# Performance work log

Hardware: AMD Instinct MI355X
Metric: run time of the kernel (lower is better)

## Reference

```python
import jax, jax.numpy as jnp
import numpy as np
from jax import lax

# ---- dims / config (see init_kwargs) ----
M_IMG, N_PCD, C = 1008, 1024, 256     # coarse img nodes (24*32+12*16+6*8), coarse pcd nodes, feat dim
NI_F, NP_F = 76800, 30000             # fine img pixels (240*320), fine pcd points
KI, KP = 64, 64                       # knn patch sizes
NUM_CORR, TOPK = 256, 3               # coarse matching params
COARSE_THR, FINE_THR = 0.0, 0.0       # similarity thresholds (lowered for random data)


def _norm(x):
    return x / (jnp.linalg.norm(x, axis=-1, keepdims=True) + 1e-8)


def setup_inputs() -> dict:
    key = jax.random.key(0)
    ks = jax.random.split(key, 7)
    return {
        "img_feats_c": _norm(jax.random.normal(ks[0], (M_IMG, C), jnp.float32)),
        "pcd_feats_c": _norm(jax.random.normal(ks[1], (N_PCD, C), jnp.float32)),
        "img_feats_f": _norm(jax.random.normal(ks[2], (NI_F, C), jnp.float32)),
        "pcd_feats_f": _norm(jax.random.normal(ks[3], (NP_F, C), jnp.float32)),
        "img_node_masks": jnp.ones((M_IMG,), bool),
        "pcd_node_masks": jnp.ones((N_PCD,), bool),
        "img_node_knn_indices": jax.random.randint(ks[4], (M_IMG, KI), 0, NI_F),
        "pcd_node_knn_indices": jax.random.randint(ks[5], (N_PCD, KP), 0, NP_F),
        "pcd_node_knn_masks": jax.random.uniform(ks[6], (N_PCD, KP)) > 0.1,
    }


def _coarse_match(img_feats_c, pcd_feats_c, img_masks, pcd_masks):
    # SuperPointMatchingMutualTopk: cosine sim + mutual top-k + global top NUM_CORR
    sim = img_feats_c @ pcd_feats_c.T                              # [M, N] (feats normalized)
    valid = img_masks[:, None] & pcd_masks[None, :]
    sim_m = jnp.where(valid, sim, -jnp.inf)
    row_kth = lax.top_k(sim_m, TOPK)[0][:, -1:]                    # kth-largest per row [M,1]
    col_kth = lax.top_k(sim_m.T, TOPK)[0][:, -1:].T                # kth-largest per col [1,N]
    mutual = (sim_m >= row_kth) & (sim_m >= col_kth) & (sim_m > COARSE_THR)
    flat = jnp.where(mutual, sim_m, -jnp.inf).ravel()
    vals, flat_idx = lax.top_k(flat, NUM_CORR)                     # fixed-size selection
    img_idx = flat_idx // N_PCD
    pcd_idx = flat_idx % N_PCD
    corr_valid = jnp.isfinite(vals)
    return img_idx, pcd_idx, corr_valid


def reference(img_feats_c, pcd_feats_c, img_feats_f, pcd_feats_f,
              img_node_masks, pcd_node_masks,
              img_node_knn_indices, pcd_node_knn_indices, pcd_node_knn_masks):
    # ---- coarse matching ----
    img_idx, pcd_idx, corr_valid = _coarse_match(
        img_feats_c, pcd_feats_c, img_node_masks, pcd_node_masks)

    # ---- fine matching: knn gather + pairwise cosine + mutual top-1 ----
    pcd_padded = jnp.concatenate([pcd_feats_f, jnp.zeros_like(pcd_feats_f[:1])], axis=0)
    img_knn_idx = img_node_knn_indices[img_idx]                    # [Ci, KI]
    pcd_knn_idx = pcd_node_knn_indices[pcd_idx]                    # [Ci, KP]
    pcd_knn_msk = pcd_node_knn_masks[pcd_idx]                      # [Ci, KP]
    img_knn_feats = img_feats_f[img_knn_idx]                       # [Ci, KI, C]
    pcd_knn_feats = pcd_padded[pcd_knn_idx]                        # [Ci, KP, C]

    sim = jnp.einsum('bic,bjc->bij', img_knn_feats, pcd_knn_feats) # [Ci, KI, KP]
    m3 = corr_valid[:, None, None] & pcd_knn_msk[:, None, :]
    sim = jnp.where(m3, sim, -jnp.inf)

    row_best = jnp.argmax(sim, axis=2)                             # [Ci, KI]
    row_val = jnp.max(sim, axis=2)
    col_best = jnp.argmax(sim, axis=1)                             # [Ci, KP]
    back = jnp.take_along_axis(col_best, row_best, axis=1)         # [Ci, KI]
    sel = (back == jnp.arange(KI)[None, :]) & jnp.isfinite(row_val) & (row_val > FINE_THR)

    img_corr = img_knn_idx.reshape(-1)                             # [Ci*KI]
    pcd_corr = jnp.take_along_axis(pcd_knn_idx, row_best, axis=1).reshape(-1)
    sel = sel.reshape(-1)
    # sentinel for unselected pairs -> sorts last
    img_corr = jnp.where(sel, img_corr, NI_F)
    pcd_corr = jnp.where(sel, pcd_corr, NP_F)

    # ---- dedup (torch.unique on img*Npf+pcd) via lexsort + first-occurrence mask ----
    order = jnp.lexsort((pcd_corr, img_corr))
    ic, pc = img_corr[order], pcd_corr[order]
    first = jnp.concatenate([jnp.array([True]),
                             (ic[1:] != ic[:-1]) | (pc[1:] != pc[:-1])])
    valid = first & (ic < NI_F)

    ic_s = jnp.clip(ic, 0, NI_F - 1)
    pc_s = jnp.clip(pc, 0, NP_F - 1)
    corr_scores = jnp.sum(img_feats_f[ic_s] * pcd_feats_f[pc_s], axis=1)
    corr_scores = corr_scores * valid.astype(corr_scores.dtype)    # masked scores [Ci*KI]
    return corr_scores
```

## Files before the change

kernel.cpp:

```cpp
#include <hip/hip_runtime.h>

#define M_IMG 1008
#define N_PCD 1024
#define CDIM  256
#define NI_F  76800
#define NP_F  30000
#define KI    64
#define KP    64
#define NUM_CORR 256
#define NPAIR (NUM_CORR * KI)
#define KEY_MOD 30001u
#define NCAND (M_IMG * 3)
#define NEG_INF (-__builtin_inff())

__device__ __forceinline__ bool mask_val(const void* p, int i, int is_u8) {
    return is_u8 ? (((const unsigned char*)p)[i] != 0)
                 : (((const int*)p)[i] != 0);
}

__device__ __forceinline__ void top3_insert(float v, float& t0, float& t1, float& t2) {
    if (v > t0) { t2 = t1; t1 = t0; t0 = v; }
    else if (v > t1) { t2 = t1; t1 = v; }
    else if (v > t2) { t2 = v; }
}

__device__ __forceinline__ void top3_merge(float a0, float a1, float a2,
                                           float b0, float b1, float b2,
                                           float& x0, float& x1, float& x2) {
    if (a0 >= b0) {
        x0 = a0;
        if (a1 >= b0) { x1 = a1; x2 = (a2 >= b0) ? a2 : b0; }
        else          { x1 = b0; x2 = (a1 >= b1) ? a1 : b1; }
    } else {
        x0 = b0;
        if (b1 >= a0) { x1 = b1; x2 = (b2 >= a0) ? b2 : a0; }
        else          { x1 = a0; x2 = (b1 >= a1) ? b1 : a1; }
    }
}

__device__ __forceinline__ void t3i_insert(float v, int i,
                                           float& v0, int& i0,
                                           float& v1, int& i1,
                                           float& v2, int& i2) {
    if (v > v0) { v2 = v1; i2 = i1; v1 = v0; i1 = i0; v0 = v; i0 = i; }
    else if (v > v1) { v2 = v1; i2 = i1; v1 = v; i1 = i; }
    else if (v > v2) { v2 = v; i2 = i; }
}

__global__ void coarse_topk_kernel(const float* __restrict__ A,
                                   const float* __restrict__ B,
                                   const void* __restrict__ maskA,
                                   const void* __restrict__ maskB,
                                   const unsigned int* __restrict__ mskw,
                                   float* __restrict__ rowp,
                                   int* __restrict__ rowpi,
                                   float* __restrict__ colp,
                                   float* __restrict__ out0,
                                   unsigned int* __restrict__ cnt,
                                   int* __restrict__ nk) {
    __shared__ __align__(16) float s_a[32][36];
    __shared__ __align__(16) float s_b[32][68];
    __shared__ float srv[32][16][3];
    __shared__ int   sri[32][16][3];
    __shared__ float scv[64][16][2];
    const int m0 = blockIdx.y * 32, n0 = blockIdx.x * 64;
    const int tid = threadIdx.x;
    const int tx = tid & 15, ty = tid >> 4;
    const int c_lane = tid & 31;
    const int r_base = tid >> 5;
    const int bx = blockIdx.x;

    const int bid = blockIdx.y * 16 + blockIdx.x;
    if (tid < 32) out0[bid * 32 + tid] = 0.f;
    if (tid >= 32 && tid < 64) cnt[bid * 32 + (tid - 32)] = 0u;
    if (bid == 0 && tid == 64) *nk = 0;

    const bool hit = (mskw[tid] & 0xFFFFFF00u) != 0u;

    const float* pa[4];
    const float* pb[8];
#pragma unroll
    for (int k = 0; k < 4; k++) {
        int m = m0 + r_base + 8 * k;
        pa[k] = A + (size_t)(m < M_IMG ? m : 0) * CDIM + c_lane;
    }
#pragma unroll
    for (int k = 0; k < 8; k++)
        pb[k] = B + (size_t)(n0 + r_base + 8 * k) * CDIM + c_lane;

    float ra[4], rb[8];
#pragma unroll
    for (int k = 0; k < 4; k++) ra[k] = pa[k][0];
#pragma unroll
    for (int k = 0; k < 8; k++) rb[k] = pb[k][0];
#pragma unroll
    for (int k = 0; k < 4; k++) s_a[c_lane][r_base + 8 * k] = ra[k];
#pragma unroll
    for (int k = 0; k < 8; k++) s_b[c_lane][r_base + 8 * k] = rb[k];
    __syncthreads();

    float acc[2][4];
#pragma unroll
    for (int r = 0; r < 2; r++)
#pragma unroll
        for (int j = 0; j < 4; j++) acc[r][j] = 0.f;

    for (int cit = 0; cit < 8; cit++) {
        if (cit < 7) {
            const int cc = (cit + 1) * 32;
#pragma unroll
            for (int k = 0; k < 4; k++) ra[k] = pa[k][cc];
#pragma unroll
            for (int k = 0; k < 8; k++) rb[k] = pb[k][cc];
        }
#pragma unroll 8
        for (int c = 0; c < 32; c++) {
            float2 av = *(const float2*)&s_a[c][ty * 2];
            float4 bv = *(const float4*)&s_b[c][tx * 4];
            float ar[2] = {av.x, av.y};
            float br[4] = {bv.x, bv.y, bv.z, bv.w};
#pragma unroll
            for (int r = 0; r < 2; r++)
#pragma unroll
                for (int j = 0; j < 4; j++) acc[r][j] += ar[r] * br[j];
        }
        __syncthreads();
        if (cit < 7) {
#pragma unroll
            for (int k = 0; k < 4; k++) s_a[c_lane][r_base + 8 * k] = ra[k];
#pragma unroll
            for (int k = 0; k < 8; k++) s_b[c_lane][r_base + 8 * k] = rb[k];
            __syncthreads();
        }
    }

    const int is_u8 = __syncthreads_or(hit ? 1 : 0);

    float mv[2][4];
#pragma unroll
    for (int r = 0; r < 2; r++) {
        int m = m0 + ty * 2 + r;
        bool ma = (m < M_IMG) ? mask_val(maskA, m, is_u8) : false;
#pragma unroll
        for (int j = 0; j < 4; j++) {
            int n = n0 + tx * 4 + j;
            bool ok = ma && mask_val(maskB, n, is_u8);
            mv[r][j] = ok ? acc[r][j] : NEG_INF;
        }
    }

#pragma unroll
    for (int r = 0; r < 2; r++) {
        float v0 = NEG_INF, v1 = NEG_INF, v2 = NEG_INF;
        int i0 = 0, i1 = 0, i2 = 0;
#pragma unroll
        for (int j = 0; j < 4; j++)
            t3i_insert(mv[r][j], n0 + tx * 4 + j, v0, i0, v1, i1, v2, i2);
        const int row = ty * 2 + r;
        srv[row][tx][0] = v0; srv[row][tx][1] = v1; srv[row][tx][2] = v2;
        sri[row][tx][0] = i0; sri[row][tx][1] = i1; sri[row][tx][2] = i2;
    }
#pragma unroll
    for (int j = 0; j < 4; j++) {
        float a = mv[0][j], b = mv[1][j];
        scv[tx * 4 + j][ty][0] = fmaxf(a, b);
        scv[tx * 4 + j][ty][1] = fminf(a, b);
    }
    __syncthreads();

    if (tid < 32) {
        const int m = m0 + tid;
        if (m < M_IMG) {
            float v0 = srv[tid][0][0], v1 = srv[tid][0][1], v2 = srv[tid][0][2];
            int   i0 = sri[tid][0][0], i1 = sri[tid][0][1], i2 = sri[tid][0][2];
            for (int t = 1; t < 16; t++)
#pragma unroll
                for (int k = 0; k < 3; k++)
                    t3i_insert(srv[tid][t][k], sri[tid][t][k],
                               v0, i0, v1, i1, v2, i2);
            const int pb0 = bx * 3;
            rowp [(pb0 + 0) * M_IMG + m] = v0; rowpi[(pb0 + 0) * M_IMG + m] = i0;
            rowp [(pb0 + 1) * M_IMG + m] = v1; rowpi[(pb0 + 1) * M_IMG + m] = i1;
            rowp [(pb0 + 2) * M_IMG + m] = v2; rowpi[(pb0 + 2) * M_IMG + m] = i2;
        }
    } else if (tid >= 64 && tid < 128) {
        const int c = tid - 64;
        float t0 = scv[c][0][0], t1 = scv[c][0][1], t2 = NEG_INF;
        for (int t = 1; t < 16; t++) {
            top3_insert(scv[c][t][0], t0, t1, t2);
            top3_insert(scv[c][t][1], t0, t1, t2);
        }
        const int n = n0 + c;
        colp[(0 * 32 + blockIdx.y) * N_PCD + n] = t0;
        colp[(1 * 32 + blockIdx.y) * N_PCD + n] = t1;
        colp[(2 * 32 + blockIdx.y) * N_PCD + n] = t2;
    }
}

__global__ __launch_bounds__(1024)
void select_kernel(const float* __restrict__ rowp,
                   const int* __restrict__ rowpi,
                   const float* __restrict__ colp,
                   int* __restrict__ sel_idx,
                   int* __restrict__ selK) {
    __shared__ float s_colk[N_PCD];
    __shared__ __align__(16) unsigned long long s_key[NCAND];
    __shared__ int s_part[1024];
    __shared__ int s_wsum[16];
    const int tid = threadIdx.x;
    const int lane = tid & 63, w = tid >> 6;

    {
        float t0 = colp[(0 * 32 + 0) * N_PCD + tid];
        float t1 = colp[(1 * 32 + 0) * N_PCD + tid];
        float t2 = colp[(2 * 32 + 0) * N_PCD + tid];
#pragma unroll 4
        for (int ch = 1; ch < 32; ch++) {
            float b0 = colp[(0 * 32 + ch) * N_PCD + tid];
            float b1 = colp[(1 * 32 + ch) * N_PCD + tid];
            float b2 = colp[(2 * 32 + ch) * N_PCD + tid];
            float x0, x1, x2;
            top3_merge(t0, t1, t2, b0, b1, b2, x0, x1, x2);
            t0 = x0; t1 = x1; t2 = x2;
        }
        s_colk[tid] = t2;
    }
    __syncthreads();

    unsigned long long kk[3] = {0, 0, 0};
    int ff[3] = {0, 0, 0};
    if (tid < M_IMG) {
        float rv[3]; int ri[3];
        rv[0] = rowp[0 * M_IMG + tid]; ri[0] = rowpi[0 * M_IMG + tid];
        rv[1] = rowp[1 * M_IMG + tid]; ri[1] = rowpi[1 * M_IMG + tid];
        rv[2] = rowp[2 * M_IMG + tid]; ri[2] = rowpi[2 * M_IMG + tid];
        for (int bx = 1; bx < 16; bx++)
#pragma unroll
            for (int s = 0; s < 3; s++)
                t3i_insert(rowp[(bx * 3 + s) * M_IMG + tid],
                           rowpi[(bx * 3 + s) * M_IMG + tid],
                           rv[0], ri[0], rv[1], ri[1], rv[2], ri[2]);
#pragma unroll
        for (int s = 0; s < 3; s++) {
            float v = rv[s]; int n = ri[s];
            if (v > 0.f && v >= s_colk[n]) {
                unsigned int u = __float_as_uint(v);
                unsigned int mono = (u & 0x80000000u) ? ~u : (u | 0x80000000u);
                kk[s] = ((unsigned long long)(~mono) << 32)
                      | (unsigned int)(tid * N_PCD + n);
                ff[s] = 1;
            }
        }
    }
    const int c = ff[0] + ff[1] + ff[2];

    int v = c;
#pragma unroll
    for (int d = 1; d < 64; d <<= 1) {
        int o = __shfl_up(v, d);
        if (lane >= d) v += o;
    }
    if (lane == 63) s_wsum[w] = v;
    __syncthreads();
    if (w == 0) {
        int x = (lane < 16) ? s_wsum[lane] : 0;
#pragma unroll
        for (int d = 1; d < 16; d <<= 1) {
            int o = __shfl_up(x, d);
            if (lane >= d) x += o;
        }
        if (lane < 16) s_wsum[lane] = x;
    }
    __syncthreads();
    const int K = s_wsum[15];
    int pos = v - c + (w > 0 ? s_wsum[w - 1] : 0);

    if (ff[0]) s_key[pos++] = kk[0];
    if (ff[1]) s_key[pos++] = kk[1];
    if (ff[2]) s_key[pos++] = kk[2];
    __syncthreads();

    if (blockIdx.x == 0 && tid == 0) *selK = (K < NUM_CORR) ? K : NUM_CORR;

    const int ii = tid & 255, q = tid >> 8;
    const int i = blockIdx.x * 256 + ii;
    const unsigned long long my = (i < K) ? s_key[i] : 0xFFFFFFFFFFFFFFFFull;
    int less = 0;
    for (int j = q; j < K; j += 4)
        less += (s_key[j] < my);
    s_part[tid] = less;
    __syncthreads();
    if (q == 0 && i < K) {
        int rank = s_part[ii] + s_part[ii + 256] + s_part[ii + 512] + s_part[ii + 768];
        if (rank < NUM_CORR)
            sel_idx[rank] = (int)(s_key[i] & 0xFFFFFFFFull);
    }
}

__global__ void fine_kernel(const float* __restrict__ img_f,
                            const float* __restrict__ pcd_f,
                            const int* __restrict__ img_knn,
                            const int* __restrict__ pcd_knn,
                            const void* __restrict__ pcd_msk,
                            const unsigned int* __restrict__ mskw,
                            const int* __restrict__ sel_idx,
                            const int* __restrict__ selK_ptr,
                            int* __restrict__ nk,
                            unsigned int* __restrict__ ckeys,
                            float* __restrict__ cscore) {
    const int ci = blockIdx.x, tid = threadIdx.x;
    if (ci >= *selK_ptr) return;
    __shared__ int s_ik[KI], s_pk[KP];
    __shared__ unsigned char s_mk[KP];
    __shared__ __align__(16) float s_a[32][68];
    __shared__ __align__(16) float s_b[32][68];
    __shared__ float s_sim[64][65];
    __shared__ int s_rb[64], s_cb[64];
    __shared__ float s_rv[64];

    const bool hit = (mskw[tid & 255] & 0xFFFFFF00u) != 0u;
    int flat = sel_idx[ci];
    int gi = flat >> 10, pi = flat & 1023;
    if (tid < 64) {
        s_ik[tid] = img_knn[gi * KI + tid];
        s_pk[tid] = pcd_knn[pi * KP + tid];
    }
    const int is_u8 = __syncthreads_or(hit ? 1 : 0);
    if (tid < 64)
        s_mk[tid] = mask_val(pcd_msk, pi * KP + tid, is_u8) ? 1 : 0;

    const int tx = tid & 15, tyy = tid >> 4;
    const int c_lane = tid & 31;
    const int r_base = tid >> 5;

    const float* pa[4];
    const float* pb[4];
#pragma unroll
    for (int k = 0; k < 4; k++) {
        pa[k] = img_f + (size_t)s_ik[r_base + 16 * k] * CDIM + c_lane;
        pb[k] = pcd_f + (size_t)s_pk[r_base + 16 * k] * CDIM + c_lane;
    }

    float ra[4], rb[4];
#pragma unroll
    for (int k = 0; k < 4; k++) { ra[k] = pa[k][0]; rb[k] = pb[k][0]; }
#pragma unroll
    for (int k = 0; k < 4; k++) {
        s_a[c_lane][r_base + 16 * k] = ra[k];
        s_b[c_lane][r_base + 16 * k] = rb[k];
    }
    __syncthreads();

    float acc[2][4];
#pragma unroll
    for (int r = 0; r < 2; r++)
#pragma unroll
        for (int j = 0; j < 4; j++) acc[r][j] = 0.f;

    for (int cit = 0; cit < 8; cit++) {
        if (cit < 7) {
            const int cc = (cit + 1) * 32;
#pragma unroll
            for (int k = 0; k < 4; k++) { ra[k] = pa[k][cc]; rb[k] = pb[k][cc]; }
        }
#pragma unroll 8
        for (int c = 0; c < 32; c++) {
            float2 av = *(const float2*)&s_a[c][tyy * 2];
            float4 bv = *(const float4*)&s_b[c][tx * 4];
            float ar[2] = {av.x, av.y};
            float br[4] = {bv.x, bv.y, bv.z, bv.w};
#pragma unroll
            for (int r = 0; r < 2; r++)
#pragma unroll
                for (int j = 0; j < 4; j++) acc[r][j] += ar[r] * br[j];
        }
        __syncthreads();
        if (cit < 7) {
#pragma unroll
            for (int k = 0; k < 4; k++) {
                s_a[c_lane][r_base + 16 * k] = ra[k];
                s_b[c_lane][r_base + 16 * k] = rb[k];
            }
            __syncthreads();
        }
    }
#pragma unroll
    for (int r = 0; r < 2; r++) {
        int row = tyy * 2 + r;
#pragma unroll
        for (int j = 0; j < 4; j++) {
            int kp = tx * 4 + j;
            s_sim[row][kp] = (s_mk[kp] != 0) ? acc[r][j] : NEG_INF;
        }
    }
    __syncthreads();

    if (tid < 64) {
        float best = NEG_INF; int bi = 0;
        for (int kp = 0; kp < 64; kp++) {
            float v = s_sim[tid][kp];
            if (v > best) { best = v; bi = kp; }
        }
        s_rb[tid] = bi; s_rv[tid] = best;
    } else if (tid < 128) {
        int kp = tid - 64;
        float best = NEG_INF; int bi = 0;
        for (int k2 = 0; k2 < 64; k2++) {
            float v = s_sim[k2][kp];
            if (v > best) { best = v; bi = k2; }
        }
        s_cb[kp] = bi;
    }
    __syncthreads();

    if (tid < 64) {
        int rb2 = s_rb[tid];
        float rv = s_rv[tid];
        if ((s_cb[rb2] == tid) && (rv > 0.f)) {
            int ik = s_ik[tid];
            int pk = s_pk[rb2];
            unsigned int key = (unsigned int)ik * KEY_MOD + (unsigned int)pk;
            const float4* a = (const float4*)(img_f + (size_t)ik * CDIM);
            const float4* b = (const float4*)(pcd_f + (size_t)pk * CDIM);
            float s = 0.f;
#pragma unroll 8
            for (int c = 0; c < CDIM / 4; c++) {
                float4 x = a[c], y = b[c];
                s += x.x * y.x + x.y * y.y + x.z * y.z + x.w * y.w;
            }
            int pos = atomicAdd(nk, 1);
            ckeys[pos] = key;
            cscore[pos] = s;
        }
    }
}

__global__ void rank_count_kernel(const unsigned int* __restrict__ ckeys,
                                  const int* __restrict__ nk,
                                  unsigned int* __restrict__ cnt) {
    const int K = *nk;
    const int bi = blockIdx.x, bj = blockIdx.y;
    if (bi * 256 >= K || bj * 256 >= K) return;
    __shared__ unsigned int s_k[256];
    const int tid = threadIdx.x;
    const int i = bi * 256 + tid;
    const unsigned int myKey = (i < K) ? ckeys[i] : 0xFFFFFFFFu;
    const int j = bj * 256 + tid;
    s_k[tid] = (j < K) ? ckeys[j] : 0xFFFFFFFFu;
    __syncthreads();

    unsigned int less = 0, eqb = 0;
    if (bj < bi) {
#pragma unroll 8
        for (int t = 0; t < 256; t++) {
            unsigned int k = s_k[t];
            less += (k < myKey);
            eqb += (k == myKey);
        }
    } else if (bj == bi) {
#pragma unroll 8
        for (int t = 0; t < 256; t++) {
            unsigned int k = s_k[t];
            less += (k < myKey);
            eqb += (k == myKey) & (t < tid);
        }
    } else {
#pragma unroll 8
        for (int t = 0; t < 256; t++) {
            unsigned int k = s_k[t];
            less += (k < myKey);
        }
    }
    unsigned int v = (less << 16) | eqb;
    if (i < K && v) atomicAdd(&cnt[i], v);
}

__global__ void rank_out_kernel(const unsigned int* __restrict__ cnt,
                                const float* __restrict__ cscore,
                                const int* __restrict__ nk,
                                float* __restrict__ out) {
    const int K = *nk;
    const int i = blockIdx.x * 256 + threadIdx.x;
    if (i >= K) return;
    const unsigned int v = cnt[i];
    if ((v & 0xFFFFu) == 0)
        out[v >> 16] = cscore[i];
}

extern "C" void kernel_launch(void* const* d_in, const int* in_sizes, int n_in,
                              void* d_out, int out_size, void* d_ws, size_t ws_size,
                              hipStream_t stream) {
    const float* img_c = (const float*)d_in[0];
    const float* pcd_c = (const float*)d_in[1];
    const float* img_f = (const float*)d_in[2];
    const float* pcd_f = (const float*)d_in[3];
    const void* img_mask = d_in[4];
    const void* pcd_mask = d_in[5];
    const int* img_knn = (const int*)d_in[6];
    const int* pcd_knn = (const int*)d_in[7];
    const void* pcd_knn_msk = d_in[8];
    float* out = (float*)d_out;

    char* w = (char*)d_ws;
    size_t off = 0;
    float* rowp = (float*)(w + off);           off += 16 * 3 * M_IMG * 4;
    int* rowpi = (int*)(w + off);              off += 16 * 3 * M_IMG * 4;
    float* colp = (float*)(w + off);           off += 3 * 32 * N_PCD * 4;
    int* sel_idx = (int*)(w + off);            off += NUM_CORR * 4;
    int* selK = (int*)(w + off);               off += 4;
    int* nk = (int*)(w + off);                 off += 4;
    unsigned int* ckeys = (unsigned int*)(w + off); off += NPAIR * 4;
    float* cscore = (float*)(w + off);         off += NPAIR * 4;
    unsigned int* cnt = (unsigned int*)(w + off);   off += NPAIR * 4;

    const unsigned int* mskw = (const unsigned int*)pcd_knn_msk;

    coarse_topk_kernel<<<dim3(16, 32), 256, 0, stream>>>(
        img_c, pcd_c, img_mask, pcd_mask, mskw, rowp, rowpi, colp, out, cnt, nk);
    select_kernel<<<12, 1024, 0, stream>>>(rowp, rowpi, colp, sel_idx, selK);
    fine_kernel<<<NUM_CORR, 512, 0, stream>>>(img_f, pcd_f, img_knn, pcd_knn,
                                              pcd_knn_msk, mskw, sel_idx, selK,
                                              nk, ckeys, cscore);
    rank_count_kernel<<<dim3(64, 64), 256, 0, stream>>>(ckeys, nk, cnt);
    rank_out_kernel<<<64, 256, 0, stream>>>(cnt, cscore, nk, out);
}
```

Measured before the change: 311.5 us.

## Split top-k partial merges into a separate parallel merge kernel

Adds a merge_kernel that reduces the per-tile row top-3 and column top-3 partials across 32 blocks, with four threads per row or column plus a shared-memory combine. Previously each of the 12 select_kernel blocks redid the full serial merge over 16 and 32 partials. select_kernel now only reads the merged values. This removes redundant serial work but adds an extra kernel launch and an extra round trip through global memory.

```diff
diff --git a/kernel.cpp b/kernel.cpp
--- a/kernel.cpp
+++ b/kernel.cpp
@@ -197,10 +197,76 @@
     }
 }
 
+__global__ void merge_kernel(const float* __restrict__ rowp,
+                             const int* __restrict__ rowpi,
+                             const float* __restrict__ colp,
+                             float* __restrict__ rowv3,
+                             int* __restrict__ rowi3,
+                             float* __restrict__ col_kth) {
+    __shared__ float sv[4][64][3];
+    __shared__ int   si[4][64][3];
+    const int tid = threadIdx.x;
+    const int lane = tid & 63, qq = tid >> 6;
+    if (blockIdx.x < 16) {
+        const int m = blockIdx.x * 64 + lane;
+        float v0 = NEG_INF, v1 = NEG_INF, v2 = NEG_INF;
+        int i0 = 0, i1 = 0, i2 = 0;
+        if (m < M_IMG) {
+#pragma unroll
+            for (int k = 0; k < 4; k++) {
+                const int sx = qq * 4 + k;
+#pragma unroll
+                for (int s = 0; s < 3; s++)
+                    t3i_insert(rowp[(sx * 3 + s) * M_IMG + m],
+                               rowpi[(sx * 3 + s) * M_IMG + m],
+                               v0, i0, v1, i1, v2, i2);
+            }
+        }
+        sv[qq][lane][0] = v0; sv[qq][lane][1] = v1; sv[qq][lane][2] = v2;
+        si[qq][lane][0] = i0; si[qq][lane][1] = i1; si[qq][lane][2] = i2;
+        __syncthreads();
+        if (qq == 0 && m < M_IMG) {
+            for (int q = 1; q < 4; q++)
+#pragma unroll
+                for (int s = 0; s < 3; s++)
+                    t3i_insert(sv[q][lane][s], si[q][lane][s],
+                               v0, i0, v1, i1, v2, i2);
+            rowv3[m * 3 + 0] = v0; rowi3[m * 3 + 0] = i0;
+            rowv3[m * 3 + 1] = v1; rowi3[m * 3 + 1] = i1;
+            rowv3[m * 3 + 2] = v2; rowi3[m * 3 + 2] = i2;
+        }
+    } else {
+        const int n = (blockIdx.x - 16) * 64 + lane;
+        float t0 = NEG_INF, t1 = NEG_INF, t2 = NEG_INF;
+#pragma unroll
+        for (int k = 0; k < 8; k++) {
+            const int ch = qq * 8 + k;
+            float b0 = colp[(0 * 32 + ch) * N_PCD + n];
+            float b1 = colp[(1 * 32 + ch) * N_PCD + n];
+            float b2 = colp[(2 * 32 + ch) * N_PCD + n];
+            float x0, x1, x2;
+            top3_merge(t0, t1, t2, b0, b1, b2, x0, x1, x2);
+            t0 = x0; t1 = x1; t2 = x2;
+        }
+        sv[qq][lane][0] = t0; sv[qq][lane][1] = t1; sv[qq][lane][2] = t2;
+        __syncthreads();
+        if (qq == 0) {
+            for (int q = 1; q < 4; q++) {
+                float x0, x1, x2;
+                top3_merge(t0, t1, t2,
+                           sv[q][lane][0], sv[q][lane][1], sv[q][lane][2],
+                           x0, x1, x2);
+                t0 = x0; t1 = x1; t2 = x2;
+            }
+            col_kth[n] = t2;
+        }
+    }
+}
+
 __global__ __launch_bounds__(1024)
-void select_kernel(const float* __restrict__ rowp,
-                   const int* __restrict__ rowpi,
-                   const float* __restrict__ colp,
+void select_kernel(const float* __restrict__ rowv3,
+                   const int* __restrict__ rowi3,
+                   const float* __restrict__ col_kth,
                    int* __restrict__ sel_idx,
                    int* __restrict__ selK) {
     __shared__ float s_colk[N_PCD];
@@ -210,49 +276,29 @@
     const int tid = threadIdx.x;
     const int lane = tid & 63, w = tid >> 6;
 
-    {
-        float t0 = colp[(0 * 32 + 0) * N_PCD + tid];
-        float t1 = colp[(1 * 32 + 0) * N_PCD + tid];
-        float t2 = colp[(2 * 32 + 0) * N_PCD + tid];
-#pragma unroll 4
-        for (int ch = 1; ch < 32; ch++) {
-            float b0 = colp[(0 * 32 + ch) * N_PCD + tid];
-            float b1 = colp[(1 * 32 + ch) * N_PCD + tid];
-            float b2 = colp[(2 * 32 + ch) * N_PCD + tid];
-            float x0, x1, x2;
-            top3_merge(t0, t1, t2, b0, b1, b2, x0, x1, x2);
-            t0 = x0; t1 = x1; t2 = x2;
-        }
-        s_colk[tid] = t2;
-    }
-    __syncthreads();
-
-    unsigned long long kk[3] = {0, 0, 0};
-    int ff[3] = {0, 0, 0};
+    s_colk[tid] = col_kth[tid];
+    __syncthreads();
+
+    unsigned long long k0 = 0, k1 = 0, k2 = 0;
+    int f0 = 0, f1 = 0, f2 = 0;
     if (tid < M_IMG) {
-        float rv[3]; int ri[3];
-        rv[0] = rowp[0 * M_IMG + tid]; ri[0] = rowpi[0 * M_IMG + tid];
-        rv[1] = rowp[1 * M_IMG + tid]; ri[1] = rowpi[1 * M_IMG + tid];
-        rv[2] = rowp[2 * M_IMG + tid]; ri[2] = rowpi[2 * M_IMG + tid];
-        for (int bx = 1; bx < 16; bx++)
-#pragma unroll
-            for (int s = 0; s < 3; s++)
-                t3i_insert(rowp[(bx * 3 + s) * M_IMG + tid],
-                           rowpi[(bx * 3 + s) * M_IMG + tid],
-                           rv[0], ri[0], rv[1], ri[1], rv[2], ri[2]);
 #pragma unroll
         for (int s = 0; s < 3; s++) {
-            float v = rv[s]; int n = ri[s];
+            float v = rowv3[tid * 3 + s];
+            int n = rowi3[tid * 3 + s];
             if (v > 0.f && v >= s_colk[n]) {
                 unsigned int u = __float_as_uint(v);
                 unsigned int mono = (u & 0x80000000u) ? ~u : (u | 0x80000000u);
-                kk[s] = ((unsigned long long)(~mono) << 32)
-                      | (unsigned int)(tid * N_PCD + n);
-                ff[s] = 1;
+                unsigned long long key =
+                    ((unsigned long long)(~mono) << 32)
+                    | (unsigned int)(tid * N_PCD + n);
+                if (s == 0) { k0 = key; f0 = 1; }
+                else if (s == 1) { k1 = key; f1 = 1; }
+                else { k2 = key; f2 = 1; }
             }
         }
     }
-    const int c = ff[0] + ff[1] + ff[2];
+    const int c = f0 + f1 + f2;
 
     int v = c;
 #pragma unroll
@@ -275,9 +321,9 @@
     const int K = s_wsum[15];
     int pos = v - c + (w > 0 ? s_wsum[w - 1] : 0);
 
-    if (ff[0]) s_key[pos++] = kk[0];
-    if (ff[1]) s_key[pos++] = kk[1];
-    if (ff[2]) s_key[pos++] = kk[2];
+    if (f0) s_key[pos++] = k0;
+    if (f1) s_key[pos++] = k1;
+    if (f2) s_key[pos++] = k2;
     __syncthreads();
 
     if (blockIdx.x == 0 && tid == 0) *selK = (K < NUM_CORR) ? K : NUM_CORR;
@@ -506,6 +552,9 @@
     float* rowp = (float*)(w + off);           off += 16 * 3 * M_IMG * 4;
     int* rowpi = (int*)(w + off);              off += 16 * 3 * M_IMG * 4;
     float* colp = (float*)(w + off);           off += 3 * 32 * N_PCD * 4;
+    float* rowv3 = (float*)(w + off);          off += M_IMG * 3 * 4;
+    int* rowi3 = (int*)(w + off);              off += M_IMG * 3 * 4;
+    float* col_kth = (float*)(w + off);        off += N_PCD * 4;
     int* sel_idx = (int*)(w + off);            off += NUM_CORR * 4;
     int* selK = (int*)(w + off);               off += 4;
     int* nk = (int*)(w + off);                 off += 4;
@@ -517,7 +566,8 @@
 
     coarse_topk_kernel<<<dim3(16, 32), 256, 0, stream>>>(
         img_c, pcd_c, img_mask, pcd_mask, mskw, rowp, rowpi, colp, out, cnt, nk);
-    select_kernel<<<12, 1024, 0, stream>>>(rowp, rowpi, colp, sel_idx, selK);
+    merge_kernel<<<32, 256, 0, stream>>>(rowp, rowpi, colp, rowv3, rowi3, col_kth);
+    select_kernel<<<12, 1024, 0, stream>>>(rowv3, rowi3, col_kth, sel_idx, selK);
     fine_kernel<<<NUM_CORR, 512, 0, stream>>>(img_f, pcd_f, img_knn, pcd_knn,
                                               pcd_knn_msk, mskw, sel_idx, selK,
                                               nk, ckeys, cscore);
```

Result: faster. 261.8 us (-16.0%).
